# Kernel optimization log

Hardware: AMD Instinct MI355X
Metric: run time of the kernel (lower is better)

The kernel has to match this reference:

```python
import jax, jax.numpy as jnp
import numpy as np

VOCAB, D, K = 100000, 300, 5

def setup_inputs() -> dict:
    key = jax.random.key(0)
    ks = jax.random.split(key, 12)
    B, BAG, L = 64, 16, 128
    token_ids = jax.random.randint(ks[0], (B * BAG, L), 0, VOCAB)
    mention_rep = jax.random.normal(ks[1], (B, BAG, D), dtype=jnp.float32)
    s = 0.05
    emb = jax.random.normal(ks[2], (VOCAB, D), dtype=jnp.float32)
    W1 = jax.random.normal(ks[3], (D, D), dtype=jnp.float32) * s
    b1 = jnp.zeros((D,), jnp.float32)
    conv_w = jax.random.normal(ks[4], (D, D, K), dtype=jnp.float32) * s  # [out, in, k]
    conv_b = jnp.zeros((D,), jnp.float32)
    W2 = jax.random.normal(ks[5], (2 * D, D), dtype=jnp.float32) * s
    b2 = jnp.zeros((D,), jnp.float32)
    W3 = jax.random.normal(ks[6], (D, D), dtype=jnp.float32) * s
    b3 = jnp.zeros((D,), jnp.float32)
    return {"token_ids": token_ids, "mention_rep": mention_rep, "emb": emb,
            "W1": W1, "b1": b1, "conv_w": conv_w, "conv_b": conv_b,
            "W2": W2, "b2": b2, "W3": W3, "b3": b3}

def reference(token_ids, mention_rep, emb, W1, b1, conv_w, conv_b, W2, b2, W3, b3):
    # fused gather+pad: [N, L, D]
    x = emb[token_ids]
    # lin1
    x = x @ W1 + b1
    # conv1d over time, VALID, stride 1: NCH layout
    xc = jnp.transpose(x, (0, 2, 1))  # [N, D, L]
    y = jax.lax.conv_general_dilated(xc, conv_w, (1,), 'VALID',
                                     dimension_numbers=('NCH', 'OIH', 'NCH'))
    y = y + conv_b[None, :, None]
    cnn_out = jnp.max(y, axis=-1)  # [N, D]
    m = mention_rep.reshape(mention_rep.shape[0] * mention_rep.shape[1], -1)  # dropout = identity (eval)
    concat = jnp.concatenate([cnn_out, m], axis=-1)
    h = jnp.tanh(concat @ W2 + b2)
    out = h @ W3 + b3  # dropout = identity (eval)
    return out
```

## Files before the change

### kernel.cpp

```cpp
#include <hip/hip_runtime.h>


#define DD   300
#define LL   128
#define TOUT 124
#define CH   16
#define XR   20
#define NSTG 8
#define BLK  320
#define KS     19
#define SLABP  6080
#define ROWP   20
#define WS_G1_OFF  0
#define WS_CV_OFF  231040
#define WS_NEEDED  1386240

typedef __attribute__((ext_vector_type(8))) _Float16 f16x8;
typedef __attribute__((ext_vector_type(4))) _Float16 f16x4;
typedef __attribute__((ext_vector_type(4))) float f32x4;
typedef unsigned int   u32;
typedef unsigned short u16;
typedef __attribute__((ext_vector_type(4))) u32 u32x4;

__device__ __forceinline__ float b2f(u16 u) {
    union { float f; u32 i; } x; x.i = ((u32)u) << 16; return x.f;
}
__device__ __forceinline__ u16 f2bu(float f) {
    union { float f; u32 i; } x; x.f = f;
    u32 r = x.i + 0x7FFFu + ((x.i >> 16) & 1u);
    return (u16)(r >> 16);
}
__device__ __forceinline__ float ld(const void* p, size_t idx, int is32) {
    return is32 ? ((const float*)p)[idx] : b2f(((const u16*)p)[idx]);
}
__device__ __forceinline__ int sniff_is32(const void* W1) {
    int cnt = 0;
    const u32* w1raw = (const u32*)W1;
    for (int i = 0; i < 64; ++i) {
        u32 e = (w1raw[i] >> 7) & 0xFFu;
        cnt += (e >= 100u && e <= 126u) ? 1 : 0;
    }
    return (cnt < 32) ? 1 : 0;
}

__device__ __forceinline__ void barrier_lgkm() {
    asm volatile("s_waitcnt lgkmcnt(0)" ::: "memory");
    __builtin_amdgcn_s_barrier();
}
__device__ __forceinline__ void barrier_only() {
    __builtin_amdgcn_s_barrier();
}

__device__ __forceinline__ void unit_decomp(int u, int& o, int& kq) {
    kq = (u >= 912) ? 3 : (u >= 608) ? 2 : (u >= 304) ? 1 : 0;
    o  = u - 304 * kq;
}

__device__ __forceinline__ void g1_load(const float* W1f, int kk, int o, int kq, float r[4]) {
    const int kbase = kk * 16 + kq * 4;
    #pragma unroll
    for (int j = 0; j < 4; ++j) {
        const int k = kbase + j;
        r[j] = (k < DD && o < DD) ? W1f[(size_t)k * DD + o] : 0.f;
    }
}
__device__ __forceinline__ void g1_write(_Float16* Ws, int o, int kq, const float r[4]) {
    f16x4 v;
    #pragma unroll
    for (int j = 0; j < 4; ++j) v[j] = (_Float16)r[j];
    *(f16x4*)&Ws[o * ROWP + (kq << 2)] = v;
}
__device__ __forceinline__ void cv_load(const float* CWf, int kk, int o, int kq, float r[20]) {
    const int kbase = kk * 16 + kq * 4;
    const bool ok = (o < DD) && (kbase < DD);
    const float4* src = (const float4*)(CWf + (size_t)o * 1500 + kk * 80 + kq * 20);
    #pragma unroll
    for (int i = 0; i < 5; ++i) {
        float4 t = ok ? src[i] : float4{0.f, 0.f, 0.f, 0.f};
        r[4*i] = t.x; r[4*i+1] = t.y; r[4*i+2] = t.z; r[4*i+3] = t.w;
    }
}
__device__ __forceinline__ void cv_write(_Float16* Ws, int o, int kq, const float r[20]) {
    #pragma unroll
    for (int s = 0; s < 5; ++s) {
        f16x4 v;
        #pragma unroll
        for (int j = 0; j < 4; ++j) v[j] = (_Float16)r[j * 5 + s];
        *(f16x4*)&Ws[s * SLABP + o * ROWP + (kq << 2)] = v;
    }
}

__global__ void CNNEncoder_36258113912977_xform(
    const void* W1, const void* conv_w, void* ws)
{
    if (!sniff_is32(W1)) return;
    const int kk = blockIdx.x, part = blockIdx.y, tid = threadIdx.x;
    const float* W1f = (const float*)W1;
    const float* CWf = (const float*)conv_w;

    if (part == 0) {
        _Float16* g1 = (_Float16*)((char*)ws + WS_G1_OFF) + (size_t)kk * SLABP;
        for (int u = tid; u < 1216; u += 512) {
            int o, kq; unit_decomp(u, o, kq);
            const int kbase = kk * 16 + (kq << 2);
            f16x4 v;
            #pragma unroll
            for (int j = 0; j < 4; ++j) {
                const int k = kbase + j;
                v[j] = (_Float16)((k < DD && o < DD) ? W1f[(size_t)k * DD + o] : 0.f);
            }
            *(f16x4*)&g1[o * ROWP + (kq << 2)] = v;
        }
    } else {
        const int s = part - 1;
        _Float16* cv = (_Float16*)((char*)ws + WS_CV_OFF) + (size_t)kk * (5 * SLABP);
        for (int u = tid; u < 1216; u += 512) {
            int o, kq; unit_decomp(u, o, kq);
            const int kbase = kk * 16 + (kq << 2);
            f16x4 v;
            #pragma unroll
            for (int j = 0; j < 4; ++j) {
                const int k = kbase + j;
                v[j] = (_Float16)((k < DD && o < DD)
                        ? CWf[(size_t)o * 1500 + (size_t)k * 5 + s] : 0.f);
            }
            *(f16x4*)&cv[s * SLABP + o * ROWP + (kq << 2)] = v;
        }
    }
}

__global__ __launch_bounds__(512, 2) void CNNEncoder_36258113912977_kernel(
    const int* __restrict__ tok, const void* mention, const void* emb,
    const void* W1, const void* b1, const void* conv_w, const void* conv_b,
    const void* W2, const void* b2, const void* W3, const void* b3,
    void* out, const void* ws)
{
    if (!sniff_is32(W1)) return;

    __shared__ __align__(16) _Float16 XB[132 * 320];
    __shared__ __align__(16) _Float16 Ws[5 * SLABP];
    __shared__ float pmax2[2][304];
    __shared__ float cbuf[2 * DD];
    __shared__ float hbuf[DD];

    const int n = blockIdx.x, tid = threadIdx.x;
    const int w   = tid >> 6;
    const int l   = tid & 63;
    const int l15 = l & 15, lg = l >> 4;
    const int wm  = w >> 2;
    const int wn  = w & 3;
    const int ntw   = (wn < 3) ? 5 : 4;
    const int nbase = wn * 80;
    const int mrow0 = wm * 64;
    const int* trow = tok + (size_t)n * LL;

    const u32x4* wsG1 = (const u32x4*)((const char*)ws + WS_G1_OFF);
    const u32x4* wsCV = (const u32x4*)((const char*)ws + WS_CV_OFF);
    u32x4* WsV = (u32x4*)Ws;
    const bool hasb  = tid < 248;
    const bool has8  = tid < 216;

    for (int i = tid; i < 132 * 160; i += 512) ((u32*)XB)[i] = 0u;
    __syncthreads();

    {
        const int r = tid >> 2, q = tid & 3;
        const float* erow = (const float*)emb + (size_t)trow[r] * DD;
        for (int c = q; c < 38; c += 4) {
            f16x8 v;
            if (c < 37) {
                const float4 f0 = *(const float4*)(erow + 8 * c);
                const float4 f1 = *(const float4*)(erow + 8 * c + 4);
                v[0]=(_Float16)f0.x; v[1]=(_Float16)f0.y;
                v[2]=(_Float16)f0.z; v[3]=(_Float16)f0.w;
                v[4]=(_Float16)f1.x; v[5]=(_Float16)f1.y;
                v[6]=(_Float16)f1.z; v[7]=(_Float16)f1.w;
            } else {
                const float4 f0 = *(const float4*)(erow + 296);
                v[0]=(_Float16)f0.x; v[1]=(_Float16)f0.y;
                v[2]=(_Float16)f0.z; v[3]=(_Float16)f0.w;
                v[4]=(_Float16)0.f; v[5]=(_Float16)0.f;
                v[6]=(_Float16)0.f; v[7]=(_Float16)0.f;
            }
            const int p = c ^ (r & 7);
            *(f16x8*)&XB[r * 320 + (p << 3)] = v;
        }
    }

    f32x4 acc[4][5];
    const f32x4 vzero = {0.f, 0.f, 0.f, 0.f};
    #pragma unroll
    for (int mt = 0; mt < 4; ++mt)
        #pragma unroll
        for (int nt = 0; nt < 5; ++nt) acc[mt][nt] = vzero;

    u32x4 sa, sb;
    u32x4 cs[8];

    {
        const u32x4* src = wsG1;
        sa = src[tid];
        if (hasb) sb = src[512 + tid];
    }
    __syncthreads();

    for (int kk = 0; kk < KS; ++kk) {
        WsV[tid] = sa;
        if (hasb) WsV[512 + tid] = sb;
        barrier_lgkm();
        if (kk + 1 < KS) {
            const u32x4* src = wsG1 + (size_t)(kk + 1) * 760;
            sa = src[tid];
            if (hasb) sb = src[512 + tid];
        } else {
            const u32x4* src = wsCV;
            #pragma unroll
            for (int p = 0; p < 7; ++p) cs[p] = src[tid + 512 * p];
            if (has8) cs[7] = src[tid + 3584];
        }
        {
            f16x4 af[4];
            #pragma unroll
            for (int mt = 0; mt < 4; ++mt) {
                const int row = mrow0 + mt * 16 + l15;
                const int c = (kk << 1) + (lg >> 1);
                af[mt] = *(const f16x4*)&XB[row * 320 + ((c ^ (row & 7)) << 3) + ((lg & 1) << 2)];
            }
            __builtin_amdgcn_s_setprio(1);
            #pragma unroll
            for (int nt = 0; nt < 5; ++nt) {
                if (nt < ntw) {
                    const int nn = nbase + nt * 16 + l15;
                    const f16x4 b = *(const f16x4*)&Ws[nn * ROWP + (lg << 2)];
                    #pragma unroll
                    for (int mt = 0; mt < 4; ++mt)
                        acc[mt][nt] = __builtin_amdgcn_mfma_f32_16x16x16f16(af[mt], b, acc[mt][nt], 0, 0, 0);
                }
            }
            __builtin_amdgcn_s_setprio(0);
        }
        barrier_only();
    }

    {
        const float* b1f = (const float*)b1;
        #pragma unroll
        for (int nt = 0; nt < 5; ++nt) {
            if (nt < ntw) {
                const int col = nbase + nt * 16 + l15;
                const float bb = (col < DD) ? b1f[col] : 0.f;
                #pragma unroll
                for (int mt = 0; mt < 4; ++mt) {
                    #pragma unroll
                    for (int j = 0; j < 4; ++j) {
                        const int row = mrow0 + mt * 16 + (lg << 2) + j;
                        XB[row * 320 + (((col >> 3) ^ (row & 7)) << 3) + (col & 7)]
                            = (_Float16)(acc[mt][nt][j] + bb);
                    }
                }
            }
        }
    }

    #pragma unroll
    for (int mt = 0; mt < 4; ++mt)
        #pragma unroll
        for (int nt = 0; nt < 5; ++nt) acc[mt][nt] = vzero;

    for (int kk = 0; kk < KS; ++kk) {
        #pragma unroll
        for (int p = 0; p < 7; ++p) WsV[tid + 512 * p] = cs[p];
        if (has8) WsV[tid + 3584] = cs[7];
        barrier_lgkm();
        if (kk + 1 < KS) {
            const u32x4* src = wsCV + (size_t)(kk + 1) * 3800;
            #pragma unroll
            for (int p = 0; p < 7; ++p) cs[p] = src[tid + 512 * p];
            if (has8) cs[7] = src[tid + 3584];
        }
        #pragma unroll
        for (int s = 0; s < 5; ++s) {
            f16x4 af[4];
            #pragma unroll
            for (int mt = 0; mt < 4; ++mt) {
                const int row = mrow0 + mt * 16 + l15 + s;
                const int c = (kk << 1) + (lg >> 1);
                af[mt] = *(const f16x4*)&XB[row * 320 + ((c ^ (row & 7)) << 3) + ((lg & 1) << 2)];
            }
            __builtin_amdgcn_s_setprio(1);
            #pragma unroll
            for (int nt = 0; nt < 5; ++nt) {
                if (nt < ntw) {
                    const int nn = nbase + nt * 16 + l15;
                    const f16x4 b = *(const f16x4*)&Ws[s * SLABP + nn * ROWP + (lg << 2)];
                    #pragma unroll
                    for (int mt = 0; mt < 4; ++mt)
                        acc[mt][nt] = __builtin_amdgcn_mfma_f32_16x16x16f16(af[mt], b, acc[mt][nt], 0, 0, 0);
                }
            }
            __builtin_amdgcn_s_setprio(0);
        }
        barrier_only();
    }

    #pragma unroll
    for (int nt = 0; nt < 5; ++nt) {
        if (nt < ntw) {
            float m = -3.0e38f;
            #pragma unroll
            for (int mt = 0; mt < 4; ++mt) {
                #pragma unroll
                for (int j = 0; j < 4; ++j) {
                    const int t = mrow0 + mt * 16 + (lg << 2) + j;
                    if (t < TOUT) m = fmaxf(m, acc[mt][nt][j]);
                }
            }
            m = fmaxf(m, __shfl_xor(m, 16));
            m = fmaxf(m, __shfl_xor(m, 32));
            if (lg == 0) pmax2[wm][nbase + nt * 16 + l15] = m;
        }
    }
    __syncthreads();

    if (tid < DD) {
        const float m = fmaxf(pmax2[0][tid], pmax2[1][tid]);
        cbuf[tid]      = m + ((const float*)conv_b)[tid];
        cbuf[DD + tid] = ((const float*)mention)[(size_t)n * DD + tid];
    }
    __syncthreads();

    if (tid < DD) {
        const float* W2f = (const float*)W2;
        float a0 = 0.f, a1 = 0.f, a2 = 0.f, a3 = 0.f;
        for (int c = 0; c < 2 * DD; c += 4) {
            a0 += cbuf[c]     * W2f[(size_t)c * DD + tid];
            a1 += cbuf[c + 1] * W2f[(size_t)(c + 1) * DD + tid];
            a2 += cbuf[c + 2] * W2f[(size_t)(c + 2) * DD + tid];
            a3 += cbuf[c + 3] * W2f[(size_t)(c + 3) * DD + tid];
        }
        hbuf[tid] = tanhf(((const float*)b2)[tid] + (a0 + a1) + (a2 + a3));
    }
    __syncthreads();

    if (tid < DD) {
        const float* W3f = (const float*)W3;
        float a0 = 0.f, a1 = 0.f;
        for (int c = 0; c < DD; c += 2) {
            a0 += hbuf[c]     * W3f[(size_t)c * DD + tid];
            a1 += hbuf[c + 1] * W3f[(size_t)(c + 1) * DD + tid];
        }
        ((float*)out)[(size_t)n * DD + tid] = ((const float*)b3)[tid] + a0 + a1;
    }
}

__global__ __launch_bounds__(512, 2) void CNNEncoder_36258113912977_nows(
    const int* __restrict__ tok, const void* mention, const void* emb,
    const void* W1, const void* b1, const void* conv_w, const void* conv_b,
    const void* W2, const void* b2, const void* W3, const void* b3,
    void* out)
{
    if (!sniff_is32(W1)) return;

    __shared__ __align__(16) _Float16 XB[132 * 320];
    __shared__ __align__(16) _Float16 Ws[5 * SLABP];
    __shared__ float pmax2[2][304];
    __shared__ float cbuf[2 * DD];
    __shared__ float hbuf[DD];

    const int n = blockIdx.x, tid = threadIdx.x;
    const int w   = tid >> 6;
    const int l   = tid & 63;
    const int l15 = l & 15, lg = l >> 4;
    const int wm  = w >> 2;
    const int wn  = w & 3;
    const int ntw   = (wn < 3) ? 5 : 4;
    const int nbase = wn * 80;
    const int mrow0 = wm * 64;
    const int* trow = tok + (size_t)n * LL;
    const float* W1f = (const float*)W1;
    const float* CWf = (const float*)conv_w;

    int o0, kq0, o1, kq1, o2, kq2;
    unit_decomp(tid, o0, kq0);
    unit_decomp(512 + tid, o1, kq1);
    const bool act2 = (l < 24);
    unit_decomp(1024 + w * 24 + (l < 24 ? l : 0), o2, kq2);

    for (int i = tid; i < 132 * 160; i += 512) ((u32*)XB)[i] = 0u;
    __syncthreads();

    {
        const int r = tid >> 2, q = tid & 3;
        const float* erow = (const float*)emb + (size_t)trow[r] * DD;
        for (int c = q; c < 38; c += 4) {
            f16x8 v;
            if (c < 37) {
                const float4 f0 = *(const float4*)(erow + 8 * c);
                const float4 f1 = *(const float4*)(erow + 8 * c + 4);
                v[0]=(_Float16)f0.x; v[1]=(_Float16)f0.y;
                v[2]=(_Float16)f0.z; v[3]=(_Float16)f0.w;
                v[4]=(_Float16)f1.x; v[5]=(_Float16)f1.y;
                v[6]=(_Float16)f1.z; v[7]=(_Float16)f1.w;
            } else {
                const float4 f0 = *(const float4*)(erow + 296);
                v[0]=(_Float16)f0.x; v[1]=(_Float16)f0.y;
                v[2]=(_Float16)f0.z; v[3]=(_Float16)f0.w;
                v[4]=(_Float16)0.f; v[5]=(_Float16)0.f;
                v[6]=(_Float16)0.f; v[7]=(_Float16)0.f;
            }
            const int p = c ^ (r & 7);
            *(f16x8*)&XB[r * 320 + (p << 3)] = v;
        }
    }

    f32x4 acc[4][5];
    const f32x4 vzero = {0.f, 0.f, 0.f, 0.f};
    #pragma unroll
    for (int mt = 0; mt < 4; ++mt)
        #pragma unroll
        for (int nt = 0; nt < 5; ++nt) acc[mt][nt] = vzero;

    float g1a[4], g1b[4], g1c[4];
    float cfa[20], cfb[20], cfc[20];

    g1_load(W1f, 0, o0, kq0, g1a);
    g1_load(W1f, 0, o1, kq1, g1b);
    if (act2) g1_load(W1f, 0, o2, kq2, g1c);
    __syncthreads();

    for (int kk = 0; kk < KS; ++kk) {
        g1_write(Ws, o0, kq0, g1a);
        g1_write(Ws, o1, kq1, g1b);
        if (act2) g1_write(Ws, o2, kq2, g1c);
        barrier_lgkm();
        if (kk + 1 < KS) {
            g1_load(W1f, kk + 1, o0, kq0, g1a);
            g1_load(W1f, kk + 1, o1, kq1, g1b);
            if (act2) g1_load(W1f, kk + 1, o2, kq2, g1c);
        } else {
            cv_load(CWf, 0, o0, kq0, cfa);
            cv_load(CWf, 0, o1, kq1, cfb);
            if (act2) cv_load(CWf, 0, o2, kq2, cfc);
        }
        {
            f16x4 af[4];
            #pragma unroll
            for (int mt = 0; mt < 4; ++mt) {
                const int row = mrow0 + mt * 16 + l15;
                const int c = (kk << 1) + (lg >> 1);
                af[mt] = *(const f16x4*)&XB[row * 320 + ((c ^ (row & 7)) << 3) + ((lg & 1) << 2)];
            }
            #pragma unroll
            for (int nt = 0; nt < 5; ++nt) {
                if (nt < ntw) {
                    const int nn = nbase + nt * 16 + l15;
                    const f16x4 b = *(const f16x4*)&Ws[nn * ROWP + (lg << 2)];
                    #pragma unroll
                    for (int mt = 0; mt < 4; ++mt)
                        acc[mt][nt] = __builtin_amdgcn_mfma_f32_16x16x16f16(af[mt], b, acc[mt][nt], 0, 0, 0);
                }
            }
        }
        barrier_only();
    }

    {
        const float* b1f = (const float*)b1;
        #pragma unroll
        for (int nt = 0; nt < 5; ++nt) {
            if (nt < ntw) {
                const int col = nbase + nt * 16 + l15;
                const float bb = (col < DD) ? b1f[col] : 0.f;
                #pragma unroll
                for (int mt = 0; mt < 4; ++mt) {
                    #pragma unroll
                    for (int j = 0; j < 4; ++j) {
                        const int row = mrow0 + mt * 16 + (lg << 2) + j;
                        XB[row * 320 + (((col >> 3) ^ (row & 7)) << 3) + (col & 7)]
                            = (_Float16)(acc[mt][nt][j] + bb);
                    }
                }
            }
        }
    }

    #pragma unroll
    for (int mt = 0; mt < 4; ++mt)
        #pragma unroll
        for (int nt = 0; nt < 5; ++nt) acc[mt][nt] = vzero;

    for (int kk = 0; kk < KS; ++kk) {
        cv_write(Ws, o0, kq0, cfa);
        cv_write(Ws, o1, kq1, cfb);
        if (act2) cv_write(Ws, o2, kq2, cfc);
        barrier_lgkm();
        if (kk + 1 < KS) {
            cv_load(CWf, kk + 1, o0, kq0, cfa);
            cv_load(CWf, kk + 1, o1, kq1, cfb);
            if (act2) cv_load(CWf, kk + 1, o2, kq2, cfc);
        }
        #pragma unroll
        for (int s = 0; s < 5; ++s) {
            f16x4 af[4];
            #pragma unroll
            for (int mt = 0; mt < 4; ++mt) {
                const int row = mrow0 + mt * 16 + l15 + s;
                const int c = (kk << 1) + (lg >> 1);
                af[mt] = *(const f16x4*)&XB[row * 320 + ((c ^ (row & 7)) << 3) + ((lg & 1) << 2)];
            }
            #pragma unroll
            for (int nt = 0; nt < 5; ++nt) {
                if (nt < ntw) {
                    const int nn = nbase + nt * 16 + l15;
                    const f16x4 b = *(const f16x4*)&Ws[s * SLABP + nn * ROWP + (lg << 2)];
                    #pragma unroll
                    for (int mt = 0; mt < 4; ++mt)
                        acc[mt][nt] = __builtin_amdgcn_mfma_f32_16x16x16f16(af[mt], b, acc[mt][nt], 0, 0, 0);
                }
            }
        }
        barrier_only();
    }

    #pragma unroll
    for (int nt = 0; nt < 5; ++nt) {
        if (nt < ntw) {
            float m = -3.0e38f;
            #pragma unroll
            for (int mt = 0; mt < 4; ++mt) {
                #pragma unroll
                for (int j = 0; j < 4; ++j) {
                    const int t = mrow0 + mt * 16 + (lg << 2) + j;
                    if (t < TOUT) m = fmaxf(m, acc[mt][nt][j]);
                }
            }
            m = fmaxf(m, __shfl_xor(m, 16));
            m = fmaxf(m, __shfl_xor(m, 32));
            if (lg == 0) pmax2[wm][nbase + nt * 16 + l15] = m;
        }
    }
    __syncthreads();

    if (tid < DD) {
        const float m = fmaxf(pmax2[0][tid], pmax2[1][tid]);
        cbuf[tid]      = m + ((const float*)conv_b)[tid];
        cbuf[DD + tid] = ((const float*)mention)[(size_t)n * DD + tid];
    }
    __syncthreads();

    if (tid < DD) {
        const float* W2f = (const float*)W2;
        float a0 = 0.f, a1 = 0.f, a2 = 0.f, a3 = 0.f;
        for (int c = 0; c < 2 * DD; c += 4) {
            a0 += cbuf[c]     * W2f[(size_t)c * DD + tid];
            a1 += cbuf[c + 1] * W2f[(size_t)(c + 1) * DD + tid];
            a2 += cbuf[c + 2] * W2f[(size_t)(c + 2) * DD + tid];
            a3 += cbuf[c + 3] * W2f[(size_t)(c + 3) * DD + tid];
        }
        hbuf[tid] = tanhf(((const float*)b2)[tid] + (a0 + a1) + (a2 + a3));
    }
    __syncthreads();

    if (tid < DD) {
        const float* W3f = (const float*)W3;
        float a0 = 0.f, a1 = 0.f;
        for (int c = 0; c < DD; c += 2) {
            a0 += hbuf[c]     * W3f[(size_t)c * DD + tid];
            a1 += hbuf[c + 1] * W3f[(size_t)(c + 1) * DD + tid];
        }
        ((float*)out)[(size_t)n * DD + tid] = ((const float*)b3)[tid] + a0 + a1;
    }
}

__global__ void CNNEncoder_36258113912977_fallback(
    const int* tok, const void* mention, const void* emb,
    const void* W1, const void* b1, const void* conv_w, const void* conv_b,
    const void* W2, const void* b2, const void* W3, const void* b3,
    void* out)
{
    __shared__ float g[XR * DD];
    __shared__ float xh[XR * DD];
    __shared__ float concat[2 * DD];
    __shared__ float hbuf[DD];

    const int n = blockIdx.x, tid = threadIdx.x;
    const int* trow = tok + (size_t)n * LL;

    if (sniff_is32(W1)) return;
    const int is32 = 0;

    float mmax = -3.0e38f;

    for (int stage = 0; stage < NSTG; ++stage) {
        const int tbase = stage * CH;
        __syncthreads();

        for (int i = tid; i < XR * DD; i += BLK) {
            int r = i / DD, c = i - (i / DD) * DD;
            int gr = tbase + r; if (gr > 127) gr = 127;
            g[i] = ld(emb, (size_t)trow[gr] * DD + c, is32);
        }
        __syncthreads();

        if (tid < DD) {
            float acc[XR];
            #pragma unroll
            for (int r = 0; r < XR; ++r) acc[r] = 0.f;
            for (int k = 0; k < DD; ++k) {
                float wv = ld(W1, (size_t)k * DD + tid, is32);
                #pragma unroll
                for (int r = 0; r < XR; ++r) acc[r] += g[r * DD + k] * wv;
            }
            float bb = ld(b1, tid, is32);
            #pragma unroll
            for (int r = 0; r < XR; ++r) xh[r * DD + tid] = acc[r] + bb;
        }
        __syncthreads();

        if (tid < DD) {
            float y[CH];
            #pragma unroll
            for (int t = 0; t < CH; ++t) y[t] = 0.f;
            const size_t cwoff = (size_t)tid * (DD * 5);
            for (int k = 0; k < DD; ++k) {
                #pragma unroll
                for (int s = 0; s < 5; ++s) {
                    float wv = ld(conv_w, cwoff + k * 5 + s, is32);
                    #pragma unroll
                    for (int t = 0; t < CH; ++t)
                        y[t] += xh[(t + s) * DD + k] * wv;
                }
            }
            #pragma unroll
            for (int t = 0; t < CH; ++t) {
                int tt = tbase + t;
                if (tt < TOUT) mmax = fmaxf(mmax, y[t]);
            }
        }
    }

    __syncthreads();
    if (tid < DD) {
        concat[tid]      = mmax + ld(conv_b, tid, is32);
        concat[DD + tid] = ld(mention, (size_t)n * DD + tid, is32);
    }
    __syncthreads();

    if (tid < DD) {
        float a = ld(b2, tid, is32);
        for (int c = 0; c < 2 * DD; ++c)
            a += concat[c] * ld(W2, (size_t)c * DD + tid, is32);
        hbuf[tid] = tanhf(a);
    }
    __syncthreads();

    if (tid < DD) {
        float a = ld(b3, tid, is32);
        for (int c = 0; c < DD; ++c)
            a += hbuf[c] * ld(W3, (size_t)c * DD + tid, is32);
        ((u16*)out)[(size_t)n * DD + tid] = f2bu(a);
    }
}

extern "C" void kernel_launch(void* const* d_in, const int* in_sizes, int n_in,
                              void* d_out, int out_size, void* d_ws, size_t ws_size,
                              hipStream_t stream)
{
    if (ws_size >= (size_t)WS_NEEDED && d_ws != nullptr) {
        CNNEncoder_36258113912977_xform<<<dim3(19, 6), 512, 0, stream>>>(
            d_in[3], d_in[5], d_ws);
        CNNEncoder_36258113912977_kernel<<<1024, 512, 0, stream>>>(
            (const int*)d_in[0], d_in[1], d_in[2], d_in[3], d_in[4], d_in[5],
            d_in[6], d_in[7], d_in[8], d_in[9], d_in[10], d_out, d_ws);
    } else {
        CNNEncoder_36258113912977_nows<<<1024, 512, 0, stream>>>(
            (const int*)d_in[0], d_in[1], d_in[2], d_in[3], d_in[4], d_in[5],
            d_in[6], d_in[7], d_in[8], d_in[9], d_in[10], d_out);
    }
    CNNEncoder_36258113912977_fallback<<<1024, BLK, 0, stream>>>(
        (const int*)d_in[0], d_in[1], d_in[2], d_in[3], d_in[4], d_in[5],
        d_in[6], d_in[7], d_in[8], d_in[9], d_in[10], d_out);
}
```

Baseline: 550.9 us.

## Switch lin1 and conv GEMMs to 32x32x16 MFMA with repacked weight layout

Replaces the 16x16x16 f16 MFMA tiling (each wave 64 rows x 80 cols) with 32x32x16 MFMA (each wave 32 rows x 160 cols, 5 accumulators of 16 floats). The workspace weight layout changes from padded rows of stride 20 to packed 8-element groups per k-half, shrinking the staged slabs and the global-to-LDS copy. The intent is fewer MFMA issues and fewer LDS fragment loads per k-step, since each A fragment is loaded once instead of four times. The max-reduction over time is rewritten for the new accumulator layout across four row-groups, with the padded rows past 124 masked.

Measured after the change: 462.3 us. 1.19x faster.

```diff
diff --git a/kernel.cpp b/kernel.cpp
--- a/kernel.cpp
+++ b/kernel.cpp
@@ -12,12 +12,13 @@
 #define SLABP  6080
 #define ROWP   20
 #define WS_G1_OFF  0
-#define WS_CV_OFF  231040
-#define WS_NEEDED  1386240
+#define WS_CV_OFF  194560
+#define WS_NEEDED  1167360
 
 typedef __attribute__((ext_vector_type(8))) _Float16 f16x8;
 typedef __attribute__((ext_vector_type(4))) _Float16 f16x4;
 typedef __attribute__((ext_vector_type(4))) float f32x4;
+typedef __attribute__((ext_vector_type(16))) float f32x16;
 typedef unsigned int   u32;
 typedef unsigned short u16;
 typedef __attribute__((ext_vector_type(4))) u32 u32x4;
@@ -55,7 +56,6 @@
     kq = (u >= 912) ? 3 : (u >= 608) ? 2 : (u >= 304) ? 1 : 0;
     o  = u - 304 * kq;
 }
-
 __device__ __forceinline__ void g1_load(const float* W1f, int kk, int o, int kq, float r[4]) {
     const int kbase = kk * 16 + kq * 4;
     #pragma unroll
@@ -95,36 +95,36 @@
 {
     if (!sniff_is32(W1)) return;
     const int kk = blockIdx.x, part = blockIdx.y, tid = threadIdx.x;
-    const float* W1f = (const float*)W1;
-    const float* CWf = (const float*)conv_w;
 
     if (part == 0) {
-        _Float16* g1 = (_Float16*)((char*)ws + WS_G1_OFF) + (size_t)kk * SLABP;
-        for (int u = tid; u < 1216; u += 512) {
-            int o, kq; unit_decomp(u, o, kq);
-            const int kbase = kk * 16 + (kq << 2);
-            f16x4 v;
-            #pragma unroll
-            for (int j = 0; j < 4; ++j) {
-                const int k = kbase + j;
-                v[j] = (_Float16)((k < DD && o < DD) ? W1f[(size_t)k * DD + o] : 0.f);
-            }
-            *(f16x4*)&g1[o * ROWP + (kq << 2)] = v;
+        const float* W1f = (const float*)W1;
+        f16x8* dst = (f16x8*)((char*)ws + WS_G1_OFF) + (size_t)kk * 640;
+        for (int g = tid; g < 640; g += 512) {
+            const int kc = (g >= 320) ? 1 : 0;
+            const int nn = g - kc * 320;
+            f16x8 v;
+            #pragma unroll
+            for (int e = 0; e < 8; ++e) {
+                const int k = kk * 16 + kc * 8 + e;
+                v[e] = (_Float16)((k < DD && nn < DD) ? W1f[(size_t)k * DD + nn] : 0.f);
+            }
+            dst[g] = v;
         }
     } else {
         const int s = part - 1;
-        _Float16* cv = (_Float16*)((char*)ws + WS_CV_OFF) + (size_t)kk * (5 * SLABP);
-        for (int u = tid; u < 1216; u += 512) {
-            int o, kq; unit_decomp(u, o, kq);
-            const int kbase = kk * 16 + (kq << 2);
-            f16x4 v;
-            #pragma unroll
-            for (int j = 0; j < 4; ++j) {
-                const int k = kbase + j;
-                v[j] = (_Float16)((k < DD && o < DD)
-                        ? CWf[(size_t)o * 1500 + (size_t)k * 5 + s] : 0.f);
-            }
-            *(f16x4*)&cv[s * SLABP + o * ROWP + (kq << 2)] = v;
+        const float* CWf = (const float*)conv_w;
+        f16x8* dst = (f16x8*)((char*)ws + WS_CV_OFF) + (size_t)kk * 3200 + (size_t)s * 640;
+        for (int g = tid; g < 640; g += 512) {
+            const int kc = (g >= 320) ? 1 : 0;
+            const int nn = g - kc * 320;
+            f16x8 v;
+            #pragma unroll
+            for (int e = 0; e < 8; ++e) {
+                const int k = kk * 16 + kc * 8 + e;
+                v[e] = (_Float16)((k < DD && nn < DD)
+                        ? CWf[(size_t)nn * 1500 + (size_t)k * 5 + s] : 0.f);
+            }
+            dst[g] = v;
         }
     }
 }
@@ -138,27 +138,25 @@
     if (!sniff_is32(W1)) return;
 
     __shared__ __align__(16) _Float16 XB[132 * 320];
-    __shared__ __align__(16) _Float16 Ws[5 * SLABP];
-    __shared__ float pmax2[2][304];
+    __shared__ __align__(16) _Float16 Ws[25600];
+    __shared__ float pmax4[4][320];
     __shared__ float cbuf[2 * DD];
     __shared__ float hbuf[DD];
 
     const int n = blockIdx.x, tid = threadIdx.x;
     const int w   = tid >> 6;
     const int l   = tid & 63;
-    const int l15 = l & 15, lg = l >> 4;
-    const int wm  = w >> 2;
-    const int wn  = w & 3;
-    const int ntw   = (wn < 3) ? 5 : 4;
-    const int nbase = wn * 80;
-    const int mrow0 = wm * 64;
+    const int l31 = l & 31, lh = l >> 5;
+    const int wm  = w >> 1;
+    const int wn  = w & 1;
+    const int nbase = wn * 160;
+    const int mrow0 = wm * 32;
     const int* trow = tok + (size_t)n * LL;
 
-    const u32x4* wsG1 = (const u32x4*)((const char*)ws + WS_G1_OFF);
-    const u32x4* wsCV = (const u32x4*)((const char*)ws + WS_CV_OFF);
-    u32x4* WsV = (u32x4*)Ws;
-    const bool hasb  = tid < 248;
-    const bool has8  = tid < 216;
+    const f16x8* wsG1 = (const f16x8*)((const char*)ws + WS_G1_OFF);
+    const f16x8* wsCV = (const f16x8*)((const char*)ws + WS_CV_OFF);
+    f16x8* WsV = (f16x8*)Ws;
+    const bool hx = (tid < 128);
 
     for (int i = tid; i < 132 * 160; i += 512) ((u32*)XB)[i] = 0u;
     __syncthreads();
@@ -187,55 +185,42 @@
         }
     }
 
-    f32x4 acc[4][5];
-    const f32x4 vzero = {0.f, 0.f, 0.f, 0.f};
-    #pragma unroll
-    for (int mt = 0; mt < 4; ++mt)
-        #pragma unroll
-        for (int nt = 0; nt < 5; ++nt) acc[mt][nt] = vzero;
-
-    u32x4 sa, sb;
-    u32x4 cs[8];
-
-    {
-        const u32x4* src = wsG1;
-        sa = src[tid];
-        if (hasb) sb = src[512 + tid];
-    }
-    __syncthreads();
-
-    for (int kk = 0; kk < KS; ++kk) {
+    f32x16 acc[5];
+    #pragma unroll
+    for (int nt = 0; nt < 5; ++nt)
+        #pragma unroll
+        for (int j = 0; j < 16; ++j) acc[nt][j] = 0.f;
+
+    f16x8 sa, sb;
+    f16x8 cs[7];
+
+    sa = wsG1[tid];
+    if (hx) sb = wsG1[512 + tid];
+    __syncthreads();
+
+    for (int kk = 0; kk < 19; ++kk) {
         WsV[tid] = sa;
-        if (hasb) WsV[512 + tid] = sb;
+        if (hx) WsV[512 + tid] = sb;
         barrier_lgkm();
-        if (kk + 1 < KS) {
-            const u32x4* src = wsG1 + (size_t)(kk + 1) * 760;
+        if (kk + 1 < 19) {
+            const f16x8* src = wsG1 + (size_t)(kk + 1) * 640;
             sa = src[tid];
-            if (hasb) sb = src[512 + tid];
+            if (hx) sb = src[512 + tid];
         } else {
-            const u32x4* src = wsCV;
-            #pragma unroll
-            for (int p = 0; p < 7; ++p) cs[p] = src[tid + 512 * p];
-            if (has8) cs[7] = src[tid + 3584];
+            #pragma unroll
+            for (int p = 0; p < 6; ++p) cs[p] = wsCV[tid + 512 * p];
+            if (hx) cs[6] = wsCV[3072 + tid];
         }
         {
-            f16x4 af[4];
-            #pragma unroll
-            for (int mt = 0; mt < 4; ++mt) {
-                const int row = mrow0 + mt * 16 + l15;
-                const int c = (kk << 1) + (lg >> 1);
-                af[mt] = *(const f16x4*)&XB[row * 320 + ((c ^ (row & 7)) << 3) + ((lg & 1) << 2)];
-            }
+            const int c = 2 * kk + lh;
+            const int row = mrow0 + l31;
+            const f16x8 a = *(const f16x8*)&XB[row * 320 + ((c ^ (row & 7)) << 3)];
             __builtin_amdgcn_s_setprio(1);
             #pragma unroll
             for (int nt = 0; nt < 5; ++nt) {
-                if (nt < ntw) {
-                    const int nn = nbase + nt * 16 + l15;
-                    const f16x4 b = *(const f16x4*)&Ws[nn * ROWP + (lg << 2)];
-                    #pragma unroll
-                    for (int mt = 0; mt < 4; ++mt)
-                        acc[mt][nt] = __builtin_amdgcn_mfma_f32_16x16x16f16(af[mt], b, acc[mt][nt], 0, 0, 0);
-                }
+                const int nn = nbase + nt * 32 + l31;
+                const f16x8 b = *(const f16x8*)&Ws[lh * 2560 + nn * 8];
+                acc[nt] = __builtin_amdgcn_mfma_f32_32x32x16_f16(a, b, acc[nt], 0, 0, 0);
             }
             __builtin_amdgcn_s_setprio(0);
         }
@@ -246,57 +231,48 @@
         const float* b1f = (const float*)b1;
         #pragma unroll
         for (int nt = 0; nt < 5; ++nt) {
-            if (nt < ntw) {
-                const int col = nbase + nt * 16 + l15;
-                const float bb = (col < DD) ? b1f[col] : 0.f;
+            const int col = nbase + nt * 32 + l31;
+            const float bb = (col < DD) ? b1f[col] : 0.f;
+            const int cc = col >> 3, c7 = col & 7;
+            #pragma unroll
+            for (int q = 0; q < 4; ++q) {
                 #pragma unroll
-                for (int mt = 0; mt < 4; ++mt) {
-                    #pragma unroll
-                    for (int j = 0; j < 4; ++j) {
-                        const int row = mrow0 + mt * 16 + (lg << 2) + j;
-                        XB[row * 320 + (((col >> 3) ^ (row & 7)) << 3) + (col & 7)]
-                            = (_Float16)(acc[mt][nt][j] + bb);
-                    }
+                for (int r = 0; r < 4; ++r) {
+                    const int row = mrow0 + q * 8 + 4 * lh + r;
+                    XB[row * 320 + ((cc ^ (row & 7)) << 3) + c7]
+                        = (_Float16)(acc[nt][4 * q + r] + bb);
                 }
             }
         }
     }
 
     #pragma unroll
-    for (int mt = 0; mt < 4; ++mt)
-        #pragma unroll
-        for (int nt = 0; nt < 5; ++nt) acc[mt][nt] = vzero;
-
-    for (int kk = 0; kk < KS; ++kk) {
-        #pragma unroll
-        for (int p = 0; p < 7; ++p) WsV[tid + 512 * p] = cs[p];
-        if (has8) WsV[tid + 3584] = cs[7];
+    for (int nt = 0; nt < 5; ++nt)
+        #pragma unroll
+        for (int j = 0; j < 16; ++j) acc[nt][j] = 0.f;
+
+    for (int kk = 0; kk < 19; ++kk) {
+        #pragma unroll
+        for (int p = 0; p < 6; ++p) WsV[tid + 512 * p] = cs[p];
+        if (hx) WsV[3072 + tid] = cs[6];
         barrier_lgkm();
-        if (kk + 1 < KS) {
-            const u32x4* src = wsCV + (size_t)(kk + 1) * 3800;
-            #pragma unroll
-            for (int p = 0; p < 7; ++p) cs[p] = src[tid + 512 * p];
-            if (has8) cs[7] = src[tid + 3584];
+        if (kk + 1 < 19) {
+            const f16x8* src = wsCV + (size_t)(kk + 1) * 3200;
+            #pragma unroll
+            for (int p = 0; p < 6; ++p) cs[p] = src[tid + 512 * p];
+            if (hx) cs[6] = src[3072 + tid];
         }
         #pragma unroll
         for (int s = 0; s < 5; ++s) {
-            f16x4 af[4];
-            #pragma unroll
-            for (int mt = 0; mt < 4; ++mt) {
-                const int row = mrow0 + mt * 16 + l15 + s;
-                const int c = (kk << 1) + (lg >> 1);
-                af[mt] = *(const f16x4*)&XB[row * 320 + ((c ^ (row & 7)) << 3) + ((lg & 1) << 2)];
-            }
+            const int c = 2 * kk + lh;
+            const int row = mrow0 + l31 + s;
+            const f16x8 a = *(const f16x8*)&XB[row * 320 + ((c ^ (row & 7)) << 3)];
             __builtin_amdgcn_s_setprio(1);
             #pragma unroll
             for (int nt = 0; nt < 5; ++nt) {
-                if (nt < ntw) {
-                    const int nn = nbase + nt * 16 + l15;
-                    const f16x4 b = *(const f16x4*)&Ws[s * SLABP + nn * ROWP + (lg << 2)];
-                    #pragma unroll
-                    for (int mt = 0; mt < 4; ++mt)
-                        acc[mt][nt] = __builtin_amdgcn_mfma_f32_16x16x16f16(af[mt], b, acc[mt][nt], 0, 0, 0);
-                }
+                const int nn = nbase + nt * 32 + l31;
+                const f16x8 b = *(const f16x8*)&Ws[s * 5120 + lh * 2560 + nn * 8];
+                acc[nt] = __builtin_amdgcn_mfma_f32_32x32x16_f16(a, b, acc[nt], 0, 0, 0);
             }
             __builtin_amdgcn_s_setprio(0);
         }
@@ -305,25 +281,25 @@
 
     #pragma unroll
     for (int nt = 0; nt < 5; ++nt) {
-        if (nt < ntw) {
-            float m = -3.0e38f;
-            #pragma unroll
-            for (int mt = 0; mt < 4; ++mt) {
+        float m = -3.0e38f;
+        #pragma unroll
+        for (int q = 0; q < 4; ++q) {
+            if (!(wm == 3 && q == 3)) {
                 #pragma unroll
-                for (int j = 0; j < 4; ++j) {
-                    const int t = mrow0 + mt * 16 + (lg << 2) + j;
-                    if (t < TOUT) m = fmaxf(m, acc[mt][nt][j]);
-                }
-            }
-            m = fmaxf(m, __shfl_xor(m, 16));
-            m = fmaxf(m, __shfl_xor(m, 32));
-            if (lg == 0) pmax2[wm][nbase + nt * 16 + l15] = m;
-        }
-    }
-    __syncthreads();
-
-    if (tid < DD) {
-        const float m = fmaxf(pmax2[0][tid], pmax2[1][tid]);
+                for (int r = 0; r < 4; ++r) m = fmaxf(m, acc[nt][4 * q + r]);
+            } else if (lh == 0) {
+                #pragma unroll
+                for (int r = 0; r < 4; ++r) m = fmaxf(m, acc[nt][12 + r]);
+            }
+        }
+        m = fmaxf(m, __shfl_xor(m, 32));
+        if (lh == 0) pmax4[wm][nbase + nt * 32 + l31] = m;
+    }
+    __syncthreads();
+
+    if (tid < DD) {
+        float m = fmaxf(fmaxf(pmax4[0][tid], pmax4[1][tid]),
+                        fmaxf(pmax4[2][tid], pmax4[3][tid]));
         cbuf[tid]      = m + ((const float*)conv_b)[tid];
         cbuf[DD + tid] = ((const float*)mention)[(size_t)n * DD + tid];
     }
```
